# Optimization experiments

Measured on AMD Instinct MI355X. Metric: run time of the kernel, lower is better.

Reference implementation:

```python
import jax, jax.numpy as jnp
import numpy as np

N_HEADS = 8
D_HEAD = 16
D_IN = 128
N_NODES = 50000
N_EDGES = 600000


def setup_inputs() -> dict:
    key = jax.random.key(0)
    ks = jax.random.split(key, 7)
    x = jax.random.normal(ks[0], (N_NODES, D_IN), dtype=jnp.float32)
    edge_attr = jax.random.normal(ks[1], (N_EDGES, D_IN), dtype=jnp.float32)
    edge_index = jax.random.randint(ks[2], (2, N_EDGES), 0, N_NODES, dtype=jnp.int32)
    # Linear weights stored as [in, out] so projection is x @ W.
    s = 1.0 / np.sqrt(D_IN)
    WQ = jax.random.normal(ks[3], (D_IN, N_HEADS * D_HEAD), dtype=jnp.float32) * s
    WK = jax.random.normal(ks[4], (D_IN, N_HEADS * D_HEAD), dtype=jnp.float32) * s
    WV = jax.random.normal(ks[5], (D_IN, N_HEADS * D_HEAD), dtype=jnp.float32) * s
    WE = jax.random.normal(ks[6], (D_IN, N_HEADS * D_HEAD), dtype=jnp.float32) * s
    return {"x": x, "edge_attr": edge_attr, "edge_index": edge_index,
            "WQ": WQ, "WK": WK, "WV": WV, "WE": WE}


def reference(x, edge_attr, edge_index, WQ, WK, WV, WE):
    N = x.shape[0]
    q = (x @ WQ).reshape(N, N_HEADS, D_HEAD)
    k = (x @ WK).reshape(N, N_HEADS, D_HEAD)
    v = (x @ WV).reshape(N, N_HEADS, D_HEAD)
    e_proj = (edge_attr @ WE).reshape(-1, N_HEADS, D_HEAD)
    row, col = edge_index[0], edge_index[1]
    # per-edge gather-compute: [E, H, D]
    alpha = (k[row] * q[col]) * (1.0 / np.sqrt(D_HEAD))
    alpha = jnp.clip(alpha, -5.0, 5.0) * e_proj
    e_out = alpha  # update_edge_feats=True
    alphax = jnp.exp(jnp.clip(alpha.sum(-1, keepdims=True), -5.0, 5.0))  # [E, H, 1]
    wV = jax.ops.segment_sum(v[row] * alphax, col, num_segments=N)  # [N, H, D]
    z = jax.ops.segment_sum(alphax, col, num_segments=N)            # [N, H, 1]
    h_out = wV / (z + 1e-6)
    return h_out, e_out
```

## Files before the change

kernel.cpp:

```cpp
#include <hip/hip_runtime.h>

#define DIN 128
#define NHEADS 8
#define DHEAD 16
#define NPB 32
#define EPB 64

typedef __attribute__((ext_vector_type(8))) short short8;
typedef __attribute__((ext_vector_type(4))) float f32x4;

__device__ __forceinline__ float clip5(float x) {
    return fminf(fmaxf(x, -5.0f), 5.0f);
}

__device__ __forceinline__ unsigned short f2bf(float f) {
    unsigned u = __float_as_uint(f);
    unsigned r = (u + 0x7FFF + ((u >> 16) & 1)) >> 16;
    return (unsigned short)r;
}

__device__ __forceinline__ float b2f(unsigned short u) {
    return __uint_as_float((unsigned)u << 16);
}

__device__ __forceinline__ float bflo(unsigned u) {
    return __uint_as_float(u << 16);
}
__device__ __forceinline__ float bfhi(unsigned u) {
    return __uint_as_float(u & 0xffff0000u);
}


__device__ __forceinline__ void tile_gemm(const float xs[][DIN], int r0, int cg,
                                          const float* __restrict__ W,
                                          float4 acc[4]) {
#pragma unroll 4
    for (int kk = 0; kk < DIN; kk += 4) {
        float4 a[4];
#pragma unroll
        for (int i = 0; i < 4; ++i)
            a[i] = *(const float4*)&xs[r0 + i][kk];
#pragma unroll
        for (int t = 0; t < 4; ++t) {
            float4 w = *(const float4*)&W[(kk + t) * DIN + (cg << 2)];
#pragma unroll
            for (int i = 0; i < 4; ++i) {
                float av = ((const float*)&a[i])[t];
                acc[i].x = fmaf(av, w.x, acc[i].x);
                acc[i].y = fmaf(av, w.y, acc[i].y);
                acc[i].z = fmaf(av, w.z, acc[i].z);
                acc[i].w = fmaf(av, w.w, acc[i].w);
            }
        }
    }
}

__global__ __launch_bounds__(256) void node_proj_kernel(
    const float* __restrict__ x, const float* __restrict__ WQ,
    const float* __restrict__ WK, const float* __restrict__ WV,
    unsigned short* __restrict__ qbf, unsigned short* __restrict__ kbf,
    unsigned short* __restrict__ vbf, int N) {
    __shared__ float xs[NPB][DIN];
    const int tid = threadIdx.x;
    const int n0 = blockIdx.x * NPB;

#pragma unroll
    for (int i = 0; i < NPB * DIN / (256 * 4); ++i) {
        int idx = (tid + i * 256) * 4;
        int r = idx / DIN, c = idx % DIN;
        float4 val = make_float4(0.f, 0.f, 0.f, 0.f);
        if (n0 + r < N) val = *(const float4*)&x[(long)(n0 + r) * DIN + c];
        *(float4*)&xs[r][c] = val;
    }
    __syncthreads();

    const int cg = tid & 31;
    const int ng = tid >> 5;
    const int r0 = ng * 4;

    const float* Ws[3] = {WQ, WK, WV};
    unsigned short* outs[3] = {qbf, kbf, vbf};
#pragma unroll
    for (int m = 0; m < 3; ++m) {
        float4 acc[4] = {make_float4(0,0,0,0), make_float4(0,0,0,0),
                         make_float4(0,0,0,0), make_float4(0,0,0,0)};
        tile_gemm(xs, r0, cg, Ws[m], acc);
#pragma unroll
        for (int i = 0; i < 4; ++i) {
            int n = n0 + r0 + i;
            if (n < N) {
                ushort4 b;
                b.x = f2bf(acc[i].x); b.y = f2bf(acc[i].y);
                b.z = f2bf(acc[i].z); b.w = f2bf(acc[i].w);
                *(ushort4*)&outs[m][(long)n * DIN + (cg << 2)] = b;
            }
        }
    }
}


__global__ __launch_bounds__(256) void degree_kernel(
    const int* __restrict__ cols, int* __restrict__ deg, int E) {
    int e = blockIdx.x * 256 + threadIdx.x;
    if (e < E) atomicAdd(&deg[cols[e]], 1);
}

__global__ __launch_bounds__(256) void block_sum_kernel(
    const int* __restrict__ deg, int* __restrict__ bsum, int N) {
    __shared__ int s[256];
    int tid = threadIdx.x;
    int i = blockIdx.x * 256 + tid;
    s[tid] = (i < N) ? deg[i] : 0;
    __syncthreads();
    for (int st = 128; st > 0; st >>= 1) {
        if (tid < st) s[tid] += s[tid + st];
        __syncthreads();
    }
    if (tid == 0) bsum[blockIdx.x] = s[0];
}

__global__ __launch_bounds__(256) void scan_bsum_kernel(int* __restrict__ bsum, int NB) {
    __shared__ int s[256];
    int tid = threadIdx.x;
    int v = (tid < NB) ? bsum[tid] : 0;
    s[tid] = v;
    __syncthreads();
    for (int off = 1; off < 256; off <<= 1) {
        int t = (tid >= off) ? s[tid - off] : 0;
        __syncthreads();
        s[tid] += t;
        __syncthreads();
    }
    if (tid < NB) bsum[tid] = s[tid] - v;
}

__global__ __launch_bounds__(256) void offsets_kernel(
    const int* __restrict__ deg, const int* __restrict__ bsumscan,
    int* __restrict__ offsets, int* __restrict__ cursor, int N, int E) {
    __shared__ int s[256];
    int tid = threadIdx.x;
    int i = blockIdx.x * 256 + tid;
    int v = (i < N) ? deg[i] : 0;
    s[tid] = v;
    __syncthreads();
    for (int off = 1; off < 256; off <<= 1) {
        int t = (tid >= off) ? s[tid - off] : 0;
        __syncthreads();
        s[tid] += t;
        __syncthreads();
    }
    int excl = s[tid] - v + bsumscan[blockIdx.x];
    if (i < N) { offsets[i] = excl; cursor[i] = excl; }
    if (blockIdx.x == 0 && tid == 0) offsets[N] = E;
}

__global__ __launch_bounds__(256) void scatter_kernel(
    const int* __restrict__ cols, int* __restrict__ cursor,
    int* __restrict__ elist, int E) {
    int e = blockIdx.x * 256 + threadIdx.x;
    if (e >= E) return;
    int pos = atomicAdd(&cursor[cols[e]], 1);
    elist[pos] = e;
}


__global__ __launch_bounds__(256) void prep_wet_kernel(
    const float* __restrict__ WE, unsigned short* __restrict__ WEt) {
    int idx = blockIdx.x * 256 + threadIdx.x;
    int kk = idx >> 7, n = idx & 127;
    WEt[n * DIN + kk] = f2bf(WE[kk * DIN + n]);
}


__global__ __launch_bounds__(256) void edge_mfma_kernel(
    const float* __restrict__ edge_attr, const int* __restrict__ edge_index,
    const unsigned short* __restrict__ WEt, const unsigned short* __restrict__ qbf,
    const unsigned short* __restrict__ kbf, float* __restrict__ e_out,
    float* __restrict__ ax, int E) {
    const int tid = threadIdx.x;
    const int e0 = blockIdx.x * EPB;
    const int w = tid >> 6;
    const int l = tid & 63;
    const int lr = l & 15;
    const int lg = l >> 4;
    const int el = w * 16 + lr;
    const long eg = e0 + el;
    const int er = edge_index[eg];
    const int ec = edge_index[E + eg];

    const float* arow = &edge_attr[eg * DIN + lg * 8];
    float4 ea[8];
#pragma unroll
    for (int ks = 0; ks < 4; ++ks) {
        ea[ks * 2]     = *(const float4*)&arow[ks * 32];
        ea[ks * 2 + 1] = *(const float4*)&arow[ks * 32 + 4];
    }
    const unsigned short* krow = &kbf[(long)er * DIN + lg * 4];
    const unsigned short* qrow = &qbf[(long)ec * DIN + lg * 4];
    ushort4 kv[8], qv[8];
#pragma unroll
    for (int ft = 0; ft < 8; ++ft) {
        kv[ft] = *(const ushort4*)&krow[ft * 16];
        qv[ft] = *(const ushort4*)&qrow[ft * 16];
    }
    __builtin_amdgcn_sched_barrier(0);

    short8 bfrag[4];
#pragma unroll
    for (int ks = 0; ks < 4; ++ks) {
        float4 a0 = ea[ks * 2], a1 = ea[ks * 2 + 1];
        short8 f;
        f[0] = (short)f2bf(a0.x); f[1] = (short)f2bf(a0.y);
        f[2] = (short)f2bf(a0.z); f[3] = (short)f2bf(a0.w);
        f[4] = (short)f2bf(a1.x); f[5] = (short)f2bf(a1.y);
        f[6] = (short)f2bf(a1.z); f[7] = (short)f2bf(a1.w);
        bfrag[ks] = f;
    }

#pragma unroll
    for (int ft = 0; ft < 8; ++ft) {
        f32x4 acc = (f32x4){0.f, 0.f, 0.f, 0.f};
#pragma unroll
        for (int ks = 0; ks < 4; ++ks) {
            short8 af = *(const short8*)&WEt[(ft * 16 + lr) * DIN + ks * 32 + lg * 8];
            acc = __builtin_amdgcn_mfma_f32_16x16x32_bf16(af, bfrag[ks], acc, 0, 0, 0);
        }
        const int f0 = ft * 16 + lg * 4;
        float4 t;
        t.x = clip5(b2f(kv[ft].x) * b2f(qv[ft].x) * 0.25f) * acc[0];
        t.y = clip5(b2f(kv[ft].y) * b2f(qv[ft].y) * 0.25f) * acc[1];
        t.z = clip5(b2f(kv[ft].z) * b2f(qv[ft].z) * 0.25f) * acc[2];
        t.w = clip5(b2f(kv[ft].w) * b2f(qv[ft].w) * 0.25f) * acc[3];
        *(float4*)&e_out[eg * DIN + f0] = t;

        float s = t.x + t.y + t.z + t.w;
        s += __shfl_xor(s, 16);
        s += __shfl_xor(s, 32);
        float axv = __expf(clip5(s));
        if (lg == 0)
            ax[eg * NHEADS + ft] = axv;
    }
}


__global__ __launch_bounds__(256) void aggregate_kernel(
    const int* __restrict__ offsets, const int* __restrict__ elist,
    const int* __restrict__ rows, const float* __restrict__ ax,
    const unsigned short* __restrict__ vbf, float* __restrict__ h_out, int N) {
    int wid = blockIdx.x * 4 + (threadIdx.x >> 6);
    int lane = threadIdx.x & 63;
    if (wid >= N) return;
    int beg = offsets[wid], end = offsets[wid + 1];
    const int head = lane >> 3;

    float2 acc = make_float2(0.f, 0.f);
    float zacc = 0.f;

    for (int j = beg; j < end; j += 8) {
        int n = end - j; n = (n > 8) ? 8 : n;
        int e_[8], r_[8];
#pragma unroll
        for (int t = 0; t < 8; ++t)
            e_[t] = elist[j + ((t < n) ? t : 0)];
#pragma unroll
        for (int t = 0; t < 8; ++t)
            r_[t] = rows[e_[t]];
        float a_[8]; unsigned u_[8];
#pragma unroll
        for (int t = 0; t < 8; ++t) {
            a_[t] = (t < n) ? ax[(long)e_[t] * NHEADS + head] : 0.f;
            u_[t] = *(const unsigned*)&vbf[(long)r_[t] * DIN + lane * 2];
        }
#pragma unroll
        for (int t = 0; t < 8; ++t) {
            acc.x = fmaf(bflo(u_[t]), a_[t], acc.x);
            acc.y = fmaf(bfhi(u_[t]), a_[t], acc.y);
            zacc += a_[t];
        }
    }
    float inv = 1.0f / (zacc + 1e-6f);
    float2 res = make_float2(acc.x * inv, acc.y * inv);
    *(float2*)&h_out[(long)wid * DIN + lane * 2] = res;
}

extern "C" void kernel_launch(void* const* d_in, const int* in_sizes, int n_in,
                              void* d_out, int out_size, void* d_ws, size_t ws_size,
                              hipStream_t stream) {
    const float* x         = (const float*)d_in[0];
    const float* edge_attr = (const float*)d_in[1];
    const int*   edge_index= (const int*)d_in[2];
    const float* WQ        = (const float*)d_in[3];
    const float* WK        = (const float*)d_in[4];
    const float* WV        = (const float*)d_in[5];
    const float* WE        = (const float*)d_in[6];

    const int N = in_sizes[0] / DIN;
    const int E = in_sizes[2] / 2;
    const int NB = (N + 255) / 256;

    float* out   = (float*)d_out;
    float* h_out = out;
    float* e_out = out + (long)N * DIN;

    unsigned short* qbf = (unsigned short*)d_ws;
    unsigned short* kbf = qbf + (long)N * DIN;
    unsigned short* vbf = kbf + (long)N * DIN;
    float* ax = (float*)(vbf + (long)N * DIN);
    unsigned short* WEt = (unsigned short*)(ax + (long)E * NHEADS);
    int* ip      = (int*)(WEt + DIN * DIN);
    int* deg     = ip;
    int* cursor  = deg + N;
    int* offsets = cursor + N;
    int* bsum    = offsets + N + 1;
    int* elist   = bsum + 256;

    const int* rows = edge_index;
    const int* cols = edge_index + E;

    hipMemsetAsync(deg, 0, (size_t)N * sizeof(int), stream);

    node_proj_kernel<<<(N + NPB - 1) / NPB, 256, 0, stream>>>(x, WQ, WK, WV, qbf, kbf, vbf, N);
    prep_wet_kernel<<<DIN * DIN / 256, 256, 0, stream>>>(WE, WEt);

    degree_kernel<<<(E + 255) / 256, 256, 0, stream>>>(cols, deg, E);
    block_sum_kernel<<<NB, 256, 0, stream>>>(deg, bsum, N);
    scan_bsum_kernel<<<1, 256, 0, stream>>>(bsum, NB);
    offsets_kernel<<<NB, 256, 0, stream>>>(deg, bsum, offsets, cursor, N, E);
    scatter_kernel<<<(E + 255) / 256, 256, 0, stream>>>(cols, cursor, elist, E);

    edge_mfma_kernel<<<E / EPB, 256, 0, stream>>>(
        edge_attr, edge_index, WEt, qbf, kbf, e_out, ax, E);

    aggregate_kernel<<<(N + 3) / 4, 256, 0, stream>>>(
        offsets, elist, rows, ax, vbf, h_out, N);
}
```

Baseline: 494.7 us.

## Process edges in destination-sorted order and add nontemporal loads/stores

The scatter kernel now also writes row and column indices permuted into CSR (destination-sorted) order. The edge kernel walks edges in that sorted order, so q rows are reused across neighbouring edges, and it writes the attention weights in sorted layout. The aggregate kernel can then read rows and weights contiguously instead of going through elist indirection. The cost is that edge_attr reads and e_out writes become scattered rows, offset by nontemporal hints on those streaming accesses.

```diff
diff --git a/kernel.cpp b/kernel.cpp
--- a/kernel.cpp
+++ b/kernel.cpp
@@ -155,12 +155,16 @@
 }
 
 __global__ __launch_bounds__(256) void scatter_kernel(
-    const int* __restrict__ cols, int* __restrict__ cursor,
-    int* __restrict__ elist, int E) {
+    const int* __restrict__ rows, const int* __restrict__ cols,
+    int* __restrict__ cursor, int* __restrict__ elist,
+    int* __restrict__ rows_s, int* __restrict__ cols_s, int E) {
     int e = blockIdx.x * 256 + threadIdx.x;
     if (e >= E) return;
-    int pos = atomicAdd(&cursor[cols[e]], 1);
+    int c = cols[e];
+    int pos = atomicAdd(&cursor[c], 1);
     elist[pos] = e;
+    rows_s[pos] = rows[e];
+    cols_s[pos] = c;
 }
 
 
@@ -173,27 +177,28 @@
 
 
 __global__ __launch_bounds__(256) void edge_mfma_kernel(
-    const float* __restrict__ edge_attr, const int* __restrict__ edge_index,
+    const float* __restrict__ edge_attr, const int* __restrict__ elist,
+    const int* __restrict__ rows_s, const int* __restrict__ cols_s,
     const unsigned short* __restrict__ WEt, const unsigned short* __restrict__ qbf,
     const unsigned short* __restrict__ kbf, float* __restrict__ e_out,
-    float* __restrict__ ax, int E) {
+    float* __restrict__ ax_s, int E) {
     const int tid = threadIdx.x;
     const int e0 = blockIdx.x * EPB;
     const int w = tid >> 6;
     const int l = tid & 63;
     const int lr = l & 15;
     const int lg = l >> 4;
-    const int el = w * 16 + lr;
-    const long eg = e0 + el;
-    const int er = edge_index[eg];
-    const int ec = edge_index[E + eg];
+    const int j = e0 + w * 16 + lr;
+    const long eg = elist[j];
+    const int er = rows_s[j];
+    const int ec = cols_s[j];
 
     const float* arow = &edge_attr[eg * DIN + lg * 8];
-    float4 ea[8];
+    f32x4 ea[8];
 #pragma unroll
     for (int ks = 0; ks < 4; ++ks) {
-        ea[ks * 2]     = *(const float4*)&arow[ks * 32];
-        ea[ks * 2 + 1] = *(const float4*)&arow[ks * 32 + 4];
+        ea[ks * 2]     = __builtin_nontemporal_load((const f32x4*)&arow[ks * 32]);
+        ea[ks * 2 + 1] = __builtin_nontemporal_load((const f32x4*)&arow[ks * 32 + 4]);
     }
     const unsigned short* krow = &kbf[(long)er * DIN + lg * 4];
     const unsigned short* qrow = &qbf[(long)ec * DIN + lg * 4];
@@ -208,12 +213,12 @@
     short8 bfrag[4];
 #pragma unroll
     for (int ks = 0; ks < 4; ++ks) {
-        float4 a0 = ea[ks * 2], a1 = ea[ks * 2 + 1];
+        f32x4 a0 = ea[ks * 2], a1 = ea[ks * 2 + 1];
         short8 f;
-        f[0] = (short)f2bf(a0.x); f[1] = (short)f2bf(a0.y);
-        f[2] = (short)f2bf(a0.z); f[3] = (short)f2bf(a0.w);
-        f[4] = (short)f2bf(a1.x); f[5] = (short)f2bf(a1.y);
-        f[6] = (short)f2bf(a1.z); f[7] = (short)f2bf(a1.w);
+        f[0] = (short)f2bf(a0[0]); f[1] = (short)f2bf(a0[1]);
+        f[2] = (short)f2bf(a0[2]); f[3] = (short)f2bf(a0[3]);
+        f[4] = (short)f2bf(a1[0]); f[5] = (short)f2bf(a1[1]);
+        f[6] = (short)f2bf(a1[2]); f[7] = (short)f2bf(a1[3]);
         bfrag[ks] = f;
     }
 
@@ -226,27 +231,27 @@
             acc = __builtin_amdgcn_mfma_f32_16x16x32_bf16(af, bfrag[ks], acc, 0, 0, 0);
         }
         const int f0 = ft * 16 + lg * 4;
-        float4 t;
-        t.x = clip5(b2f(kv[ft].x) * b2f(qv[ft].x) * 0.25f) * acc[0];
-        t.y = clip5(b2f(kv[ft].y) * b2f(qv[ft].y) * 0.25f) * acc[1];
-        t.z = clip5(b2f(kv[ft].z) * b2f(qv[ft].z) * 0.25f) * acc[2];
-        t.w = clip5(b2f(kv[ft].w) * b2f(qv[ft].w) * 0.25f) * acc[3];
-        *(float4*)&e_out[eg * DIN + f0] = t;
-
-        float s = t.x + t.y + t.z + t.w;
+        f32x4 t;
+        t[0] = clip5(b2f(kv[ft].x) * b2f(qv[ft].x) * 0.25f) * acc[0];
+        t[1] = clip5(b2f(kv[ft].y) * b2f(qv[ft].y) * 0.25f) * acc[1];
+        t[2] = clip5(b2f(kv[ft].z) * b2f(qv[ft].z) * 0.25f) * acc[2];
+        t[3] = clip5(b2f(kv[ft].w) * b2f(qv[ft].w) * 0.25f) * acc[3];
+        __builtin_nontemporal_store(t, (f32x4*)&e_out[eg * DIN + f0]);
+
+        float s = t[0] + t[1] + t[2] + t[3];
         s += __shfl_xor(s, 16);
         s += __shfl_xor(s, 32);
         float axv = __expf(clip5(s));
         if (lg == 0)
-            ax[eg * NHEADS + ft] = axv;
+            ax_s[(long)j * NHEADS + ft] = axv;
     }
 }
 
 
 __global__ __launch_bounds__(256) void aggregate_kernel(
-    const int* __restrict__ offsets, const int* __restrict__ elist,
-    const int* __restrict__ rows, const float* __restrict__ ax,
-    const unsigned short* __restrict__ vbf, float* __restrict__ h_out, int N) {
+    const int* __restrict__ offsets, const int* __restrict__ rows_s,
+    const float* __restrict__ ax_s, const unsigned short* __restrict__ vbf,
+    float* __restrict__ h_out, int N) {
     int wid = blockIdx.x * 4 + (threadIdx.x >> 6);
     int lane = threadIdx.x & 63;
     if (wid >= N) return;
@@ -258,17 +263,13 @@
 
     for (int j = beg; j < end; j += 8) {
         int n = end - j; n = (n > 8) ? 8 : n;
-        int e_[8], r_[8];
+        int r_[8]; float a_[8]; unsigned u_[8];
 #pragma unroll
         for (int t = 0; t < 8; ++t)
-            e_[t] = elist[j + ((t < n) ? t : 0)];
-#pragma unroll
-        for (int t = 0; t < 8; ++t)
-            r_[t] = rows[e_[t]];
-        float a_[8]; unsigned u_[8];
+            r_[t] = rows_s[j + ((t < n) ? t : 0)];
 #pragma unroll
         for (int t = 0; t < 8; ++t) {
-            a_[t] = (t < n) ? ax[(long)e_[t] * NHEADS + head] : 0.f;
+            a_[t] = (t < n) ? ax_s[(long)(j + t) * NHEADS + head] : 0.f;
             u_[t] = *(const unsigned*)&vbf[(long)r_[t] * DIN + lane * 2];
         }
 #pragma unroll
@@ -305,14 +306,16 @@
     unsigned short* qbf = (unsigned short*)d_ws;
     unsigned short* kbf = qbf + (long)N * DIN;
     unsigned short* vbf = kbf + (long)N * DIN;
-    float* ax = (float*)(vbf + (long)N * DIN);
-    unsigned short* WEt = (unsigned short*)(ax + (long)E * NHEADS);
+    float* ax_s = (float*)(vbf + (long)N * DIN);
+    unsigned short* WEt = (unsigned short*)(ax_s + (long)E * NHEADS);
     int* ip      = (int*)(WEt + DIN * DIN);
     int* deg     = ip;
     int* cursor  = deg + N;
     int* offsets = cursor + N;
     int* bsum    = offsets + N + 1;
     int* elist   = bsum + 256;
+    int* rows_s  = elist + E;
+    int* cols_s  = rows_s + E;
 
     const int* rows = edge_index;
     const int* cols = edge_index + E;
@@ -326,11 +329,12 @@
     block_sum_kernel<<<NB, 256, 0, stream>>>(deg, bsum, N);
     scan_bsum_kernel<<<1, 256, 0, stream>>>(bsum, NB);
     offsets_kernel<<<NB, 256, 0, stream>>>(deg, bsum, offsets, cursor, N, E);
-    scatter_kernel<<<(E + 255) / 256, 256, 0, stream>>>(cols, cursor, elist, E);
+    scatter_kernel<<<(E + 255) / 256, 256, 0, stream>>>(rows, cols, cursor,
+                                                        elist, rows_s, cols_s, E);
 
     edge_mfma_kernel<<<E / EPB, 256, 0, stream>>>(
-        edge_attr, edge_index, WEt, qbf, kbf, e_out, ax, E);
+        edge_attr, elist, rows_s, cols_s, WEt, qbf, kbf, e_out, ax_s, E);
 
     aggregate_kernel<<<(N + 3) / 4, 256, 0, stream>>>(
-        offsets, elist, rows, ax, vbf, h_out, N);
-}
+        offsets, rows_s, ax_s, vbf, h_out, N);
+}
```

New measurement: 485.7 us. No clear change (-1.8%).
